# Kernel optimization log

Measured on AMD Instinct MI355X. Metric: run time of the kernel, lower is better.

## Reference

```python
import jax, jax.numpy as jnp
import numpy as np

L, B, E = 128, 16, 512
C_OUT = 64
KERNELS = [1, 3, 5, 7]
M = len(KERNELS) * C_OUT          # mlpdec_in = 256
OUT_SIZE = 256
SLOPE = 0.1


def setup_inputs() -> dict:
    key = jax.random.key(0)
    ks = jax.random.split(key, 32)
    s = 0.02
    d = {"x": jax.random.normal(ks[0], (L, B, E), dtype=jnp.float32)}
    # conv branches: weight (C_out, 1, k, E), bias (C_out,)
    for i, k in enumerate(KERNELS):
        d[f"cw{i}"] = jax.random.normal(ks[1 + 2 * i], (C_OUT, 1, k, E), dtype=jnp.float32) * s
        d[f"cb{i}"] = jnp.zeros((C_OUT,), dtype=jnp.float32)
    dims = [(C_OUT, 2 * M), (C_OUT, C_OUT), (C_OUT, C_OUT), (C_OUT, C_OUT)]
    for i, (o, inn) in enumerate(dims):
        d[f"mw{i}"] = jax.random.normal(ks[10 + 2 * i], (o, inn), dtype=jnp.float32) * s
        d[f"mb{i}"] = jnp.zeros((o,), dtype=jnp.float32)
    # mlp_layer: Linear(C->C), Linear(C->output_size)
    d["lw0"] = jax.random.normal(ks[20], (C_OUT, C_OUT), dtype=jnp.float32) * s
    d["lb0"] = jnp.zeros((C_OUT,), dtype=jnp.float32)
    d["lw1"] = jax.random.normal(ks[21], (OUT_SIZE, C_OUT), dtype=jnp.float32) * s
    d["lb1"] = jnp.zeros((OUT_SIZE,), dtype=jnp.float32)
    return d


def _lrelu(x):
    return jax.nn.leaky_relu(x, SLOPE)


def _conv_branch(xb, w, b):
    # xb: (B,1,L,E), w: (C,1,k,E) -> (B,C,L)
    k = w.shape[2]
    pad = (k - 1) // 2
    y = jax.lax.conv_general_dilated(
        xb, w, window_strides=(1, 1), padding=[(pad, pad), (0, 0)],
        dimension_numbers=("NCHW", "OIHW", "NCHW"))
    return _lrelu(y[..., 0] + b[None, :, None])


def reference(x, cw0, cb0, cw1, cb1, cw2, cb2, cw3, cb3,
              mw0, mb0, mw1, mb1, mw2, mb2, mw3, mb3,
              lw0, lb0, lw1, lb1):
    # x: (L,B,E) -> (B,1,L,E)
    xb = jnp.transpose(x, (1, 0, 2))[:, None, :, :]
    feats = jnp.concatenate([
        _conv_branch(xb, cw0, cb0), _conv_branch(xb, cw1, cb1),
        _conv_branch(xb, cw2, cb2), _conv_branch(xb, cw3, cb3)], axis=1)  # (B, 4C, L)
    f = jnp.transpose(feats, (2, 0, 1))  # (L, B, M)
    # pairwise: pair[i, j] = [f[j], f[i]]  -> (L, L, B, 2M)
    a = jnp.broadcast_to(f[None, :, :, :], (L, L, B, M))
    bpart = jnp.broadcast_to(f[:, None, :, :], (L, L, B, M))
    h = jnp.concatenate([a, bpart], axis=-1)
    for w, bb in ((mw0, mb0), (mw1, mb1), (mw2, mb2), (mw3, mb3)):
        h = _lrelu(h @ w.T + bb)
    h = h.sum(axis=0)  # (L, B, C)
    h = _lrelu(h @ lw0.T + lb0)
    return _lrelu(h @ lw1.T + lb1)  # (L, B, OUT_SIZE)
```

## Files before the change

### kernel.cpp

```cpp
#include <hip/hip_runtime.h>
#include <hip/hip_bf16.h>

#define SLOPE 0.1f
typedef unsigned short u16;
typedef unsigned int u32;
typedef __attribute__((ext_vector_type(8))) short short8;
typedef __attribute__((ext_vector_type(4))) float floatx4;

__device__ __forceinline__ float lrelu(float x) { return x > 0.0f ? x : SLOPE * x; }

__device__ __forceinline__ void split_rn(float x, u16* h, u16* l) {
    union { __hip_bfloat16 b; u16 u; } c1, c2;
    c1.b = __float2bfloat16(x);
    float hf = __bfloat162float(c1.b);
    c2.b = __float2bfloat16(x - hf);
    *h = c1.u; *l = c2.u;
}

__device__ __forceinline__ void pack2x2(float v0, float v1, u32& h, u32& l) {
    u32 a0 = __float_as_uint(v0), a1 = __float_as_uint(v1);
    h = __builtin_amdgcn_perm(a1, a0, 0x07060302u);
    float r0 = v0 - __uint_as_float(a0 & 0xFFFF0000u);
    float r1 = v1 - __uint_as_float(a1 & 0xFFFF0000u);
    l = __builtin_amdgcn_perm(__float_as_uint(r1), __float_as_uint(r0), 0x07060302u);
}

__device__ __forceinline__ short8 load_frag(const u16* p) {
    union { uint4 q; short8 s; } cv;
    cv.q = *(const uint4*)p;
    return cv.s;
}

__device__ __forceinline__ floatx4 mfma16(short8 a, short8 b, floatx4 c) {
    return __builtin_amdgcn_mfma_f32_16x16x32_bf16(a, b, c, 0, 0, 0);
}

__global__ __launch_bounds__(256) void p0_prep(
    const float* __restrict__ x,
    const float* __restrict__ cw0, const float* __restrict__ cw1,
    const float* __restrict__ cw2, const float* __restrict__ cw3,
    const float* __restrict__ mw0, const float* __restrict__ mw1,
    const float* __restrict__ mw2, const float* __restrict__ mw3,
    const float* __restrict__ lw0, const float* __restrict__ lw1,
    u16* __restrict__ xfh, u16* __restrict__ xfl,
    u16* __restrict__ wcfh, u16* __restrict__ wcfl,
    u16* __restrict__ b2fh, u16* __restrict__ b2fl,
    u16* __restrict__ w3fh, u16* __restrict__ w3fl,
    float* __restrict__ lw0t, float* __restrict__ lw1t)
{
    int idx = blockIdx.x * 256 + threadIdx.x;
    if (idx < 1048576) {
        const int j = idx & 7, lane = (idx >> 3) & 63;
        const int kc = (idx >> 9) & 15, rt = idx >> 13;
        const int l15 = lane & 15, quad = lane >> 4;
        split_rn(x[(rt * 16 + l15) * 512 + kc * 32 + quad * 8 + j], &xfh[idx], &xfl[idx]);
        return;
    }
    idx -= 1048576;
    if (idx < 524288) {
        const int j = idx & 7, lane = (idx >> 3) & 63;
        const int kc = (idx >> 9) & 15, nt = (idx >> 13) & 3, slot = idx >> 15;
        int branch, base;
        if (slot == 0)      { branch = 0; base = 0; }
        else if (slot < 4)  { branch = 1; base = 1; }
        else if (slot < 9)  { branch = 2; base = 4; }
        else                { branch = 3; base = 9; }
        const int dk = slot - base, ksz = 2 * branch + 1;
        const float* cw = branch == 0 ? cw0 : branch == 1 ? cw1 : branch == 2 ? cw2 : cw3;
        const int c = nt * 16 + (lane & 15);
        const int e = kc * 32 + (lane >> 4) * 8 + j;
        split_rn(cw[(c * ksz + dk) * 512 + e], &wcfh[idx], &wcfl[idx]);
        return;
    }
    idx -= 524288;
    if (idx < 32768) {
        const int j = idx & 7, lane = (idx >> 3) & 63;
        const int kc = (idx >> 9) & 7, nt = (idx >> 12) & 3, nh = idx >> 14;
        const int n = nh * 64 + nt * 16 + (lane & 15);
        const int k = kc * 32 + (lane >> 4) * 8 + j;
        split_rn(mw0[(n & 63) * 512 + (n >> 6) * 256 + k], &b2fh[idx], &b2fl[idx]);
        return;
    }
    idx -= 32768;
    if (idx < 12288) {
        const int j = idx & 7, lane = (idx >> 3) & 63;
        const int kc = (idx >> 9) & 1, mt = (idx >> 10) & 3, layer = idx >> 12;
        const float* mw = layer == 0 ? mw1 : layer == 1 ? mw2 : mw3;
        const int ch = mt * 16 + (lane & 15);
        const int k = kc * 32 + (lane >> 4) * 8 + j;
        split_rn(mw[ch * 64 + k], &w3fh[idx], &w3fl[idx]);
        return;
    }
    idx -= 12288;
    if (idx < 4096) { const int k = idx >> 6, n = idx & 63; lw0t[idx] = lw0[n * 64 + k]; return; }
    idx -= 4096;
    if (idx < 16384) { const int k = idx >> 8, n = idx & 255; lw1t[idx] = lw1[n * 64 + k]; return; }
}

__global__ __launch_bounds__(256) void k1f_conv(
    const u16* __restrict__ xfh, const u16* __restrict__ xfl,
    const u16* __restrict__ wcfh, const u16* __restrict__ wcfl,
    const float* __restrict__ cb0, const float* __restrict__ cb1,
    const float* __restrict__ cb2, const float* __restrict__ cb3,
    u16* __restrict__ Ffh, u16* __restrict__ Ffl)
{
    __shared__ float P[4][16][72];

    const int t = threadIdx.x, lane = t & 63, w = t >> 6;
    const int rt = blockIdx.x;
    const int br = blockIdx.y;
    const int base = br * br;
    const int ksz = 2 * br + 1;
    const int l15 = lane & 15, quad = lane >> 4;

    floatx4 acc[4];
    #pragma unroll
    for (int j = 0; j < 4; ++j) acc[j] = (floatx4)0.0f;

    const int nunits = ksz * 16;
    for (int unit = w; unit < nunits; unit += 4) {
        const int dk = unit >> 4, kc = unit & 15;
        const int rts = rt + dk - br;
        if (rts < 0 || rts >= 128) continue;
        const int aoff = ((rts * 16 + kc) * 64 + lane) * 8;
        const short8 ah = load_frag(xfh + aoff);
        const short8 al = load_frag(xfl + aoff);
        const int slot = base + dk;
        #pragma unroll
        for (int nt = 0; nt < 4; ++nt) {
            const int boff = (((slot * 4 + nt) * 16 + kc) * 64 + lane) * 8;
            const short8 bh = load_frag(wcfh + boff);
            const short8 bl = load_frag(wcfl + boff);
            acc[nt] = mfma16(ah, bh, acc[nt]);
            acc[nt] = mfma16(ah, bl, acc[nt]);
            acc[nt] = mfma16(al, bh, acc[nt]);
        }
    }

    #pragma unroll
    for (int nt = 0; nt < 4; ++nt)
        #pragma unroll
        for (int r = 0; r < 4; ++r)
            P[w][quad * 4 + r][nt * 16 + l15] = acc[nt][r];
    __syncthreads();

    const float* cb = br == 0 ? cb0 : br == 1 ? cb1 : br == 2 ? cb2 : cb3;
    const int row = t >> 4, c4 = (t & 15) * 4;
    u16 h4[4], l4[4];
    #pragma unroll
    for (int i = 0; i < 4; ++i) {
        float val = P[0][row][c4 + i] + P[1][row][c4 + i]
                  + P[2][row][c4 + i] + P[3][row][c4 + i] + cb[c4 + i];
        split_rn(lrelu(val), &h4[i], &l4[i]);
    }
    const int m4 = br * 64 + c4;
    const int dst = ((rt * 8 + (m4 >> 5)) * 64 + ((m4 >> 3) & 3) * 16 + row) * 8 + (m4 & 7);
    *(ushort4*)(Ffh + dst) = make_ushort4(h4[0], h4[1], h4[2], h4[3]);
    *(ushort4*)(Ffl + dst) = make_ushort4(l4[0], l4[1], l4[2], l4[3]);
}

__global__ __launch_bounds__(256) void k2_uv(
    const u16* __restrict__ Ffh, const u16* __restrict__ Ffl,
    const u16* __restrict__ b2fh, const u16* __restrict__ b2fl,
    const float* __restrict__ mb0,
    float* __restrict__ u, float* __restrict__ v_t)
{
    __shared__ float P[4][16][72];

    const int t = threadIdx.x, lane = t & 63, w = t >> 6;
    const int rt = blockIdx.x;
    const int nh = blockIdx.y;
    const int l15 = lane & 15, quad = lane >> 4;

    floatx4 acc[4];
    #pragma unroll
    for (int j = 0; j < 4; ++j) acc[j] = (floatx4)0.0f;

    #pragma unroll
    for (int kk = 0; kk < 2; ++kk) {
        const int kc = w * 2 + kk;
        const int aoff = ((rt * 8 + kc) * 64 + lane) * 8;
        const short8 ah = load_frag(Ffh + aoff);
        const short8 al = load_frag(Ffl + aoff);
        #pragma unroll
        for (int nt = 0; nt < 4; ++nt) {
            const int boff = (((nh * 4 + nt) * 8 + kc) * 64 + lane) * 8;
            const short8 bh = load_frag(b2fh + boff);
            const short8 bl = load_frag(b2fl + boff);
            acc[nt] = mfma16(ah, bh, acc[nt]);
            acc[nt] = mfma16(ah, bl, acc[nt]);
            acc[nt] = mfma16(al, bh, acc[nt]);
        }
    }

    #pragma unroll
    for (int nt = 0; nt < 4; ++nt)
        #pragma unroll
        for (int r = 0; r < 4; ++r)
            P[w][quad * 4 + r][nt * 16 + l15] = acc[nt][r];
    __syncthreads();

    const int row = t >> 4, c4 = (t & 15) * 4;
    const int rglob = rt * 16 + row;
    float4 oo;
    #pragma unroll
    for (int i = 0; i < 4; ++i)
        (&oo.x)[i] = P[0][row][c4 + i] + P[1][row][c4 + i]
                   + P[2][row][c4 + i] + P[3][row][c4 + i];
    if (nh == 0) {
        oo.x += mb0[c4 + 0]; oo.y += mb0[c4 + 1];
        oo.z += mb0[c4 + 2]; oo.w += mb0[c4 + 3];
        *(float4*)(u + rglob * 64 + c4) = oo;
    } else {
        const int i = rglob >> 4, b = rglob & 15;
        *(float4*)(v_t + (b * 128 + i) * 64 + c4) = oo;
    }
}

__global__ __launch_bounds__(256, 4) void k3_pair(
    const float* __restrict__ u, const float* __restrict__ v_t,
    const u16* __restrict__ w3fh, const u16* __restrict__ w3fl,
    const float* __restrict__ mb1, const float* __restrict__ mb2,
    const float* __restrict__ mb3,
    float* __restrict__ Spart)
{
    __shared__ __align__(16) u16 Hh[128][72];
    __shared__ __align__(16) u16 Hl[128][72];
    __shared__ __align__(16) float us[64];

    const int t = threadIdx.x, lane = t & 63, w = t >> 6;
    const int jb = blockIdx.x, b = jb & 15;
    const int l15 = lane & 15, quad = lane >> 4;
    const int i0 = w * 32;

    if (t < 64) us[t] = u[jb * 64 + t];
    __syncthreads();

    const float* vb = v_t + (b * 128 + i0) * 64;
    #pragma unroll
    for (int n = 0; n < 8; ++n) {
        const int idx = n * 64 + lane;
        const int il = idx >> 4, c4 = (idx & 15) * 4;
        const float4 vv = *(const float4*)(vb + idx * 4);
        const float4 uu = *(const float4*)(&us[c4]);
        const float a0 = lrelu(vv.x + uu.x), a1 = lrelu(vv.y + uu.y);
        const float a2 = lrelu(vv.z + uu.z), a3 = lrelu(vv.w + uu.w);
        u32 h01, l01, h23, l23;
        pack2x2(a0, a1, h01, l01);
        pack2x2(a2, a3, h23, l23);
        *(uint2*)&Hh[i0 + il][c4] = make_uint2(h01, h23);
        *(uint2*)&Hl[i0 + il][c4] = make_uint2(l01, l23);
    }

    const float* mbp[3] = {mb1, mb2, mb3};
    for (int layer = 0; layer < 3; ++layer) {
        floatx4 acc[4][2];
        #pragma unroll
        for (int i = 0; i < 4; ++i)
            #pragma unroll
            for (int j = 0; j < 2; ++j) acc[i][j] = (floatx4)0.0f;

        #pragma unroll
        for (int kc = 0; kc < 2; ++kc) {
            short8 ah[4], al[4];
            #pragma unroll
            for (int mt = 0; mt < 4; ++mt) {
                const int aoff = (((layer * 4 + mt) * 2 + kc) * 64 + lane) * 8;
                ah[mt] = load_frag(w3fh + aoff);
                al[mt] = load_frag(w3fl + aoff);
            }
            const int k0 = kc * 32 + quad * 8;
            #pragma unroll
            for (int nt = 0; nt < 2; ++nt) {
                const short8 bh = load_frag(&Hh[i0 + nt * 16 + l15][k0]);
                const short8 bl = load_frag(&Hl[i0 + nt * 16 + l15][k0]);
                #pragma unroll
                for (int mt = 0; mt < 4; ++mt) {
                    acc[mt][nt] = mfma16(ah[mt], bh, acc[mt][nt]);
                    acc[mt][nt] = mfma16(ah[mt], bl, acc[mt][nt]);
                    acc[mt][nt] = mfma16(al[mt], bh, acc[mt][nt]);
                }
            }
        }

        if (layer < 2) {
            #pragma unroll
            for (int mt = 0; mt < 4; ++mt) {
                float bias[4];
                #pragma unroll
                for (int r = 0; r < 4; ++r) bias[r] = mbp[layer][mt * 16 + quad * 4 + r];
                #pragma unroll
                for (int nt = 0; nt < 2; ++nt) {
                    const int i = i0 + nt * 16 + l15;
                    const float v0 = lrelu(acc[mt][nt][0] + bias[0]);
                    const float v1 = lrelu(acc[mt][nt][1] + bias[1]);
                    const float v2 = lrelu(acc[mt][nt][2] + bias[2]);
                    const float v3 = lrelu(acc[mt][nt][3] + bias[3]);
                    u32 h01, l01, h23, l23;
                    pack2x2(v0, v1, h01, l01);
                    pack2x2(v2, v3, h23, l23);
                    *(uint2*)&Hh[i][mt * 16 + quad * 4] = make_uint2(h01, h23);
                    *(uint2*)&Hl[i][mt * 16 + quad * 4] = make_uint2(l01, l23);
                }
            }
        } else {
            #pragma unroll
            for (int mt = 0; mt < 4; ++mt) {
                float bias[4];
                #pragma unroll
                for (int r = 0; r < 4; ++r) bias[r] = mbp[2][mt * 16 + quad * 4 + r];
                float4 sv;
                #pragma unroll
                for (int r = 0; r < 4; ++r) {
                    float val = lrelu(acc[mt][0][r] + bias[r])
                              + lrelu(acc[mt][1][r] + bias[r]);
                    val += __shfl_xor(val, 1, 16);
                    val += __shfl_xor(val, 2, 16);
                    val += __shfl_xor(val, 4, 16);
                    val += __shfl_xor(val, 8, 16);
                    (&sv.x)[r] = val;
                }
                if (l15 == 0)
                    *(float4*)(Spart + jb * 256 + w * 64 + mt * 16 + quad * 4) = sv;
            }
        }
    }
}

__global__ __launch_bounds__(256) void k4_head(
    const float* __restrict__ Spart,
    const float* __restrict__ lw0t, const float* __restrict__ lb0,
    const float* __restrict__ lw1t, const float* __restrict__ lb1,
    float* __restrict__ out)
{
    __shared__ float Ss[8][64];
    __shared__ float T1[8][64];

    const int t = threadIdx.x;
    const int jb0 = blockIdx.x * 8;

    #pragma unroll
    for (int p = 0; p < 2; ++p) {
        const int idx = t + 256 * p;
        const int jbb = idx >> 6, ch = idx & 63;
        const float* sp = Spart + (jb0 + jbb) * 256 + ch;
        Ss[jbb][ch] = sp[0] + sp[64] + sp[128] + sp[192];
    }
    __syncthreads();

    #pragma unroll
    for (int p = 0; p < 2; ++p) {
        const int idx = t + 256 * p;
        const int jbb = idx >> 6, c = idx & 63;
        float a = lb0[c];
        #pragma unroll 8
        for (int k = 0; k < 64; ++k) a += Ss[jbb][k] * lw0t[k * 64 + c];
        T1[jbb][c] = lrelu(a);
    }
    __syncthreads();

    const int c = t;
    float acc[8];
    const float base = lb1[c];
    #pragma unroll
    for (int jbb = 0; jbb < 8; ++jbb) acc[jbb] = base;
    #pragma unroll 4
    for (int k = 0; k < 64; ++k) {
        const float wv = lw1t[k * 256 + c];
        #pragma unroll
        for (int jbb = 0; jbb < 8; ++jbb) acc[jbb] += T1[jbb][k] * wv;
    }
    #pragma unroll
    for (int jbb = 0; jbb < 8; ++jbb)
        out[(jb0 + jbb) * 256 + c] = lrelu(acc[jbb]);
}

extern "C" void kernel_launch(void* const* d_in, const int* in_sizes, int n_in,
                              void* d_out, int out_size, void* d_ws, size_t ws_size,
                              hipStream_t stream)
{
    const float* x   = (const float*)d_in[0];
    const float* cw0 = (const float*)d_in[1];
    const float* cb0 = (const float*)d_in[2];
    const float* cw1 = (const float*)d_in[3];
    const float* cb1 = (const float*)d_in[4];
    const float* cw2 = (const float*)d_in[5];
    const float* cb2 = (const float*)d_in[6];
    const float* cw3 = (const float*)d_in[7];
    const float* cb3 = (const float*)d_in[8];
    const float* mw0 = (const float*)d_in[9];
    const float* mb0 = (const float*)d_in[10];
    const float* mw1 = (const float*)d_in[11];
    const float* mb1 = (const float*)d_in[12];
    const float* mw2 = (const float*)d_in[13];
    const float* mb2 = (const float*)d_in[14];
    const float* mw3 = (const float*)d_in[15];
    const float* mb3 = (const float*)d_in[16];
    const float* lw0 = (const float*)d_in[17];
    const float* lb0 = (const float*)d_in[18];
    const float* lw1 = (const float*)d_in[19];
    const float* lb1 = (const float*)d_in[20];
    float* out = (float*)d_out;

    char* base = (char*)d_ws;
    u16* xfh   = (u16*)(base + 0);
    u16* xfl   = (u16*)(base + 2097152);
    u16* wcfh  = (u16*)(base + 4194304);
    u16* wcfl  = (u16*)(base + 5242880);
    u16* b2fh  = (u16*)(base + 6291456);
    u16* b2fl  = (u16*)(base + 6356992);
    u16* w3fh  = (u16*)(base + 6422528);
    u16* w3fl  = (u16*)(base + 6447104);
    float* lw0t  = (float*)(base + 6471680);
    float* lw1t  = (float*)(base + 6488064);
    u16* Ffh   = (u16*)(base + 6553600);
    u16* Ffl   = (u16*)(base + 7602176);
    float* u   = (float*)(base + 8650752);
    float* v_t = (float*)(base + 9175040);
    float* Spart = (float*)(base + 9699328);

    hipLaunchKernelGGL(p0_prep, dim3(6400), dim3(256), 0, stream,
                       x, cw0, cw1, cw2, cw3, mw0, mw1, mw2, mw3, lw0, lw1,
                       xfh, xfl, wcfh, wcfl, b2fh, b2fl, w3fh, w3fl, lw0t, lw1t);
    hipLaunchKernelGGL(k1f_conv, dim3(128, 4), dim3(256), 0, stream,
                       xfh, xfl, wcfh, wcfl, cb0, cb1, cb2, cb3, Ffh, Ffl);
    hipLaunchKernelGGL(k2_uv, dim3(128, 2), dim3(256), 0, stream,
                       Ffh, Ffl, b2fh, b2fl, mb0, u, v_t);
    hipLaunchKernelGGL(k3_pair, dim3(2048), dim3(256), 0, stream,
                       u, v_t, w3fh, w3fl, mb1, mb2, mb3, Spart);
    hipLaunchKernelGGL(k4_head, dim3(256), dim3(256), 0, stream,
                       Spart, lw0t, lb0, lw1t, lb1, out);
}
```

Measured before the change: 174.8 us.

## Vectorize prep kernel, reuse conv weight fragments across two row tiles

The prep kernel now has each thread handle four consecutive elements with float4 loads and ushort4 stores, so it launches a quarter as many blocks. The conv kernel runs 512 threads per block, each covering two row tiles 64 apart. Each weight fragment is loaded once and reused for both tiles, which halves weight traffic in exchange for more registers and an extra reduction pass with barriers. The pair kernel reads its u slice straight from global memory into registers instead of staging it through shared memory with a barrier.

After: 156.8 us, median of 2. -10.3%, faster.

```diff
diff --git a/kernel.cpp b/kernel.cpp
--- a/kernel.cpp
+++ b/kernel.cpp
@@ -48,12 +48,17 @@
     u16* __restrict__ w3fh, u16* __restrict__ w3fl,
     float* __restrict__ lw0t, float* __restrict__ lw1t)
 {
-    int idx = blockIdx.x * 256 + threadIdx.x;
+    int idx = (blockIdx.x * 256 + threadIdx.x) * 4;
     if (idx < 1048576) {
         const int j = idx & 7, lane = (idx >> 3) & 63;
         const int kc = (idx >> 9) & 15, rt = idx >> 13;
         const int l15 = lane & 15, quad = lane >> 4;
-        split_rn(x[(rt * 16 + l15) * 512 + kc * 32 + quad * 8 + j], &xfh[idx], &xfl[idx]);
+        const float4 s = *(const float4*)(x + (rt * 16 + l15) * 512 + kc * 32 + quad * 8 + j);
+        u16 h[4], l[4];
+        split_rn(s.x, &h[0], &l[0]); split_rn(s.y, &h[1], &l[1]);
+        split_rn(s.z, &h[2], &l[2]); split_rn(s.w, &h[3], &l[3]);
+        *(ushort4*)(xfh + idx) = make_ushort4(h[0], h[1], h[2], h[3]);
+        *(ushort4*)(xfl + idx) = make_ushort4(l[0], l[1], l[2], l[3]);
         return;
     }
     idx -= 1048576;
@@ -69,7 +74,12 @@
         const float* cw = branch == 0 ? cw0 : branch == 1 ? cw1 : branch == 2 ? cw2 : cw3;
         const int c = nt * 16 + (lane & 15);
         const int e = kc * 32 + (lane >> 4) * 8 + j;
-        split_rn(cw[(c * ksz + dk) * 512 + e], &wcfh[idx], &wcfl[idx]);
+        const float4 s = *(const float4*)(cw + (c * ksz + dk) * 512 + e);
+        u16 h[4], l[4];
+        split_rn(s.x, &h[0], &l[0]); split_rn(s.y, &h[1], &l[1]);
+        split_rn(s.z, &h[2], &l[2]); split_rn(s.w, &h[3], &l[3]);
+        *(ushort4*)(wcfh + idx) = make_ushort4(h[0], h[1], h[2], h[3]);
+        *(ushort4*)(wcfl + idx) = make_ushort4(l[0], l[1], l[2], l[3]);
         return;
     }
     idx -= 524288;
@@ -78,7 +88,12 @@
         const int kc = (idx >> 9) & 7, nt = (idx >> 12) & 3, nh = idx >> 14;
         const int n = nh * 64 + nt * 16 + (lane & 15);
         const int k = kc * 32 + (lane >> 4) * 8 + j;
-        split_rn(mw0[(n & 63) * 512 + (n >> 6) * 256 + k], &b2fh[idx], &b2fl[idx]);
+        const float4 s = *(const float4*)(mw0 + (n & 63) * 512 + (n >> 6) * 256 + k);
+        u16 h[4], l[4];
+        split_rn(s.x, &h[0], &l[0]); split_rn(s.y, &h[1], &l[1]);
+        split_rn(s.z, &h[2], &l[2]); split_rn(s.w, &h[3], &l[3]);
+        *(ushort4*)(b2fh + idx) = make_ushort4(h[0], h[1], h[2], h[3]);
+        *(ushort4*)(b2fl + idx) = make_ushort4(l[0], l[1], l[2], l[3]);
         return;
     }
     idx -= 32768;
@@ -88,75 +103,110 @@
         const float* mw = layer == 0 ? mw1 : layer == 1 ? mw2 : mw3;
         const int ch = mt * 16 + (lane & 15);
         const int k = kc * 32 + (lane >> 4) * 8 + j;
-        split_rn(mw[ch * 64 + k], &w3fh[idx], &w3fl[idx]);
+        const float4 s = *(const float4*)(mw + ch * 64 + k);
+        u16 h[4], l[4];
+        split_rn(s.x, &h[0], &l[0]); split_rn(s.y, &h[1], &l[1]);
+        split_rn(s.z, &h[2], &l[2]); split_rn(s.w, &h[3], &l[3]);
+        *(ushort4*)(w3fh + idx) = make_ushort4(h[0], h[1], h[2], h[3]);
+        *(ushort4*)(w3fl + idx) = make_ushort4(l[0], l[1], l[2], l[3]);
         return;
     }
     idx -= 12288;
-    if (idx < 4096) { const int k = idx >> 6, n = idx & 63; lw0t[idx] = lw0[n * 64 + k]; return; }
+    if (idx < 4096) {
+        const int k = idx >> 6, n = idx & 63;
+        float4 o;
+        o.x = lw0[(n + 0) * 64 + k]; o.y = lw0[(n + 1) * 64 + k];
+        o.z = lw0[(n + 2) * 64 + k]; o.w = lw0[(n + 3) * 64 + k];
+        *(float4*)(lw0t + idx) = o;
+        return;
+    }
     idx -= 4096;
-    if (idx < 16384) { const int k = idx >> 8, n = idx & 255; lw1t[idx] = lw1[n * 64 + k]; return; }
-}
-
-__global__ __launch_bounds__(256) void k1f_conv(
+    if (idx < 16384) {
+        const int k = idx >> 8, n = idx & 255;
+        float4 o;
+        o.x = lw1[(n + 0) * 64 + k]; o.y = lw1[(n + 1) * 64 + k];
+        o.z = lw1[(n + 2) * 64 + k]; o.w = lw1[(n + 3) * 64 + k];
+        *(float4*)(lw1t + idx) = o;
+        return;
+    }
+}
+
+__global__ __launch_bounds__(512) void k1f_conv(
     const u16* __restrict__ xfh, const u16* __restrict__ xfl,
     const u16* __restrict__ wcfh, const u16* __restrict__ wcfl,
     const float* __restrict__ cb0, const float* __restrict__ cb1,
     const float* __restrict__ cb2, const float* __restrict__ cb3,
     u16* __restrict__ Ffh, u16* __restrict__ Ffl)
 {
-    __shared__ float P[4][16][72];
+    __shared__ float P[8][16][72];
 
     const int t = threadIdx.x, lane = t & 63, w = t >> 6;
-    const int rt = blockIdx.x;
+    const int rtp = blockIdx.x;
     const int br = blockIdx.y;
     const int base = br * br;
     const int ksz = 2 * br + 1;
     const int l15 = lane & 15, quad = lane >> 4;
 
-    floatx4 acc[4];
-    #pragma unroll
-    for (int j = 0; j < 4; ++j) acc[j] = (floatx4)0.0f;
+    floatx4 acc[2][4];
+    #pragma unroll
+    for (int r = 0; r < 2; ++r)
+        #pragma unroll
+        for (int j = 0; j < 4; ++j) acc[r][j] = (floatx4)0.0f;
 
     const int nunits = ksz * 16;
-    for (int unit = w; unit < nunits; unit += 4) {
+    for (int unit = w; unit < nunits; unit += 8) {
         const int dk = unit >> 4, kc = unit & 15;
-        const int rts = rt + dk - br;
-        if (rts < 0 || rts >= 128) continue;
-        const int aoff = ((rts * 16 + kc) * 64 + lane) * 8;
-        const short8 ah = load_frag(xfh + aoff);
-        const short8 al = load_frag(xfl + aoff);
         const int slot = base + dk;
+        short8 bh[4], bl[4];
         #pragma unroll
         for (int nt = 0; nt < 4; ++nt) {
             const int boff = (((slot * 4 + nt) * 16 + kc) * 64 + lane) * 8;
-            const short8 bh = load_frag(wcfh + boff);
-            const short8 bl = load_frag(wcfl + boff);
-            acc[nt] = mfma16(ah, bh, acc[nt]);
-            acc[nt] = mfma16(ah, bl, acc[nt]);
-            acc[nt] = mfma16(al, bh, acc[nt]);
-        }
-    }
-
-    #pragma unroll
-    for (int nt = 0; nt < 4; ++nt)
-        #pragma unroll
-        for (int r = 0; r < 4; ++r)
-            P[w][quad * 4 + r][nt * 16 + l15] = acc[nt][r];
-    __syncthreads();
+            bh[nt] = load_frag(wcfh + boff);
+            bl[nt] = load_frag(wcfl + boff);
+        }
+        #pragma unroll
+        for (int r = 0; r < 2; ++r) {
+            const int rts = rtp + r * 64 + dk - br;
+            if (rts < 0 || rts >= 128) continue;
+            const int aoff = ((rts * 16 + kc) * 64 + lane) * 8;
+            const short8 ah = load_frag(xfh + aoff);
+            const short8 al = load_frag(xfl + aoff);
+            #pragma unroll
+            for (int nt = 0; nt < 4; ++nt) {
+                acc[r][nt] = mfma16(ah, bh[nt], acc[r][nt]);
+                acc[r][nt] = mfma16(ah, bl[nt], acc[r][nt]);
+                acc[r][nt] = mfma16(al, bh[nt], acc[r][nt]);
+            }
+        }
+    }
 
     const float* cb = br == 0 ? cb0 : br == 1 ? cb1 : br == 2 ? cb2 : cb3;
-    const int row = t >> 4, c4 = (t & 15) * 4;
-    u16 h4[4], l4[4];
-    #pragma unroll
-    for (int i = 0; i < 4; ++i) {
-        float val = P[0][row][c4 + i] + P[1][row][c4 + i]
-                  + P[2][row][c4 + i] + P[3][row][c4 + i] + cb[c4 + i];
-        split_rn(lrelu(val), &h4[i], &l4[i]);
-    }
-    const int m4 = br * 64 + c4;
-    const int dst = ((rt * 8 + (m4 >> 5)) * 64 + ((m4 >> 3) & 3) * 16 + row) * 8 + (m4 & 7);
-    *(ushort4*)(Ffh + dst) = make_ushort4(h4[0], h4[1], h4[2], h4[3]);
-    *(ushort4*)(Ffl + dst) = make_ushort4(l4[0], l4[1], l4[2], l4[3]);
+    #pragma unroll
+    for (int r = 0; r < 2; ++r) {
+        #pragma unroll
+        for (int nt = 0; nt < 4; ++nt)
+            #pragma unroll
+            for (int rr = 0; rr < 4; ++rr)
+                P[w][quad * 4 + rr][nt * 16 + l15] = acc[r][nt][rr];
+        __syncthreads();
+        if (t < 256) {
+            const int row = t >> 4, c4 = (t & 15) * 4;
+            u16 h4[4], l4[4];
+            #pragma unroll
+            for (int i = 0; i < 4; ++i) {
+                float val = cb[c4 + i];
+                #pragma unroll
+                for (int ww = 0; ww < 8; ++ww) val += P[ww][row][c4 + i];
+                split_rn(lrelu(val), &h4[i], &l4[i]);
+            }
+            const int rt = rtp + r * 64;
+            const int m4 = br * 64 + c4;
+            const int dst = ((rt * 8 + (m4 >> 5)) * 64 + ((m4 >> 3) & 3) * 16 + row) * 8 + (m4 & 7);
+            *(ushort4*)(Ffh + dst) = make_ushort4(h4[0], h4[1], h4[2], h4[3]);
+            *(ushort4*)(Ffl + dst) = make_ushort4(l4[0], l4[1], l4[2], l4[3]);
+        }
+        __syncthreads();
+    }
 }
 
 __global__ __launch_bounds__(256) void k2_uv(
@@ -226,23 +276,21 @@
 {
     __shared__ __align__(16) u16 Hh[128][72];
     __shared__ __align__(16) u16 Hl[128][72];
-    __shared__ __align__(16) float us[64];
 
     const int t = threadIdx.x, lane = t & 63, w = t >> 6;
     const int jb = blockIdx.x, b = jb & 15;
     const int l15 = lane & 15, quad = lane >> 4;
     const int i0 = w * 32;
-
-    if (t < 64) us[t] = u[jb * 64 + t];
-    __syncthreads();
+    const int c4 = l15 * 4;
+
+    const float4 uu = *(const float4*)(u + jb * 64 + c4);
 
     const float* vb = v_t + (b * 128 + i0) * 64;
     #pragma unroll
     for (int n = 0; n < 8; ++n) {
         const int idx = n * 64 + lane;
-        const int il = idx >> 4, c4 = (idx & 15) * 4;
+        const int il = idx >> 4;
         const float4 vv = *(const float4*)(vb + idx * 4);
-        const float4 uu = *(const float4*)(&us[c4]);
         const float a0 = lrelu(vv.x + uu.x), a1 = lrelu(vv.y + uu.y);
         const float a2 = lrelu(vv.z + uu.z), a3 = lrelu(vv.w + uu.w);
         u32 h01, l01, h23, l23;
@@ -419,10 +467,10 @@
     float* v_t = (float*)(base + 9175040);
     float* Spart = (float*)(base + 9699328);
 
-    hipLaunchKernelGGL(p0_prep, dim3(6400), dim3(256), 0, stream,
+    hipLaunchKernelGGL(p0_prep, dim3(1600), dim3(256), 0, stream,
                        x, cw0, cw1, cw2, cw3, mw0, mw1, mw2, mw3, lw0, lw1,
                        xfh, xfl, wcfh, wcfl, b2fh, b2fl, w3fh, w3fl, lw0t, lw1t);
-    hipLaunchKernelGGL(k1f_conv, dim3(128, 4), dim3(256), 0, stream,
+    hipLaunchKernelGGL(k1f_conv, dim3(64, 4), dim3(512), 0, stream,
                        xfh, xfl, wcfh, wcfl, cb0, cb1, cb2, cb3, Ffh, Ffl);
     hipLaunchKernelGGL(k2_uv, dim3(128, 2), dim3(256), 0, stream,
                        Ffh, Ffl, b2fh, b2fl, mb0, u, v_t);
```
